# Optimization experiments

Hardware: AMD Instinct MI355X
Metric: run time of the kernel (lower is better)

The kernel has to match this reference:

```python
import jax, jax.numpy as jnp
import numpy as np

BATCH_K = 8
CUTOFF = 0.5
NONZERO_LOSS_CUTOFF = 1.4
N, D = 8192, 128


def setup_inputs() -> dict:
    key = jax.random.key(0)
    x = jax.random.normal(key, (N, D), dtype=jnp.float32)
    # the sqrt(2 - 2*sim) distance assumes unit-norm embeddings
    x = x / jnp.linalg.norm(x, axis=1, keepdims=True)
    return {"x": x}


def _forward(x, key):
    n, d = x.shape
    k = BATCH_K
    # pairwise distances on the unit sphere
    sim = x @ x.T                                   # [n, n]
    dist = jnp.sqrt(jnp.maximum(2.0 - 2.0 * sim, 0.0))
    # clamp distance from below at cutoff (canonical distance-weighted sampling;
    # repo's clamp(max=) + torch.maxx are typos that make the original code NaN/crash)
    dist = jnp.maximum(dist, CUTOFF)
    one_minus = jnp.maximum(1.0 - 0.25 * dist * dist, 1e-8)  # tiny clip for log safety
    log_w = (2.0 - float(d)) * jnp.log(dist) - (float(d - 3) / 2.0) * jnp.log(one_minus)
    w = jnp.exp(log_w - jnp.max(log_w))
    # zero out the same-class (block-diagonal) entries and far pairs
    blk = jnp.arange(n) // k
    neq_block = (blk[:, None] != blk[None, :]).astype(x.dtype)
    w = w * neq_block * (dist < NONZERO_LOSS_CUTOFF).astype(x.dtype)
    row_sum = jnp.sum(w, axis=1, keepdims=True)
    # uniform fallback for degenerate rows (mirrors the try/except in the original)
    probs = jnp.where(row_sum > 0, w / row_sum, 1.0 / n)   # [n, n]
    # per-row categorical sampling of k-1 negatives WITH replacement
    logits = jnp.log(probs)                                # -inf where prob==0 (ok)
    n_idx = jax.random.categorical(key, logits, shape=(k - 1, n)).T.reshape(-1)  # [n*(k-1)]
    # anchor/positive pairs: all same-block pairs (i, j), j != i
    a_idx = jnp.repeat(jnp.arange(n), k - 1)               # [n*(k-1)]
    p_mat = blk[:, None] * k + jnp.arange(k)[None, :]      # [n, k]
    keep = p_mat != jnp.arange(n)[:, None]
    order = jnp.argsort(jnp.logical_not(keep), axis=1, stable=True)
    p_idx = jnp.take_along_axis(p_mat, order, axis=1)[:, : k - 1].reshape(-1)
    return a_idx, x[a_idx], x[p_idx], x[n_idx], x


def reference(x):
    return _forward(x, jax.random.key(1))
```

## Files before the change

### kernel.cpp

```cpp
#include <hip/hip_runtime.h>

#define NN   8192
#define DD   128
#define KM1  7
#define TPB  256
#define NBLK 512

#define O0_END   57344
#define O1_END   7397376
#define O2_END   14737408
#define O3_END   22077440
#define TOTAL    23126016
#define NKEY     57344

typedef __attribute__((ext_vector_type(8))) short bf16x8;
typedef __attribute__((ext_vector_type(4))) float f32x4;

__device__ __forceinline__ unsigned mix32(unsigned h) {
  h ^= h >> 16; h *= 0x85ebca6bu; h ^= h >> 13; h *= 0xc2b2ae35u; h ^= h >> 16;
  return h;
}

__device__ __forceinline__ float wfun(float dot, int col, int rowblk) {
  float d2m = fmaxf(fmaf(-2.f, dot, 2.f), 0.25f);
  bool vb = ((col >> 3) != rowblk) && (d2m < 1.96f);
  float lgd = __log2f(d2m);
  float om  = fmaf(-0.25f, d2m, 1.f);
  float lgo = __log2f(om);
  float lgw = fmaf(-62.5f, lgo, fmaf(-63.f, lgd, -63.f));
  float w   = __builtin_amdgcn_exp2f(lgw);
  return vb ? w : 0.f;
}

__device__ __forceinline__ float wave_incl_scan(float v, int lane) {
#pragma unroll
  for (int off = 1; off < 64; off <<= 1) {
    float t = __shfl_up(v, off);
    if (lane >= off) v += t;
  }
  return v;
}

__global__ __launch_bounds__(256) void to_bf16(const float* __restrict__ x,
                                               unsigned short* __restrict__ xb,
                                               unsigned short* __restrict__ xbf) {
  const int c = blockIdx.x * 256 + threadIdx.x;
  const int l15 = c & 15, g = (c >> 4) & 3, kk = (c >> 6) & 3, R = c >> 8;
  const int row = R * 16 + l15;
  const int j0  = kk * 32 + g * 8;
  const float* src = x + (size_t)row * DD + j0;
  float4 a = *reinterpret_cast<const float4*>(src);
  float4 b = *reinterpret_cast<const float4*>(src + 4);
  unsigned short o[8];
  unsigned u;
  u = __float_as_uint(a.x); o[0] = (unsigned short)((u + 0x7FFFu + ((u >> 16) & 1u)) >> 16);
  u = __float_as_uint(a.y); o[1] = (unsigned short)((u + 0x7FFFu + ((u >> 16) & 1u)) >> 16);
  u = __float_as_uint(a.z); o[2] = (unsigned short)((u + 0x7FFFu + ((u >> 16) & 1u)) >> 16);
  u = __float_as_uint(a.w); o[3] = (unsigned short)((u + 0x7FFFu + ((u >> 16) & 1u)) >> 16);
  u = __float_as_uint(b.x); o[4] = (unsigned short)((u + 0x7FFFu + ((u >> 16) & 1u)) >> 16);
  u = __float_as_uint(b.y); o[5] = (unsigned short)((u + 0x7FFFu + ((u >> 16) & 1u)) >> 16);
  u = __float_as_uint(b.z); o[6] = (unsigned short)((u + 0x7FFFu + ((u >> 16) & 1u)) >> 16);
  u = __float_as_uint(b.w); o[7] = (unsigned short)((u + 0x7FFFu + ((u >> 16) & 1u)) >> 16);
  bf16x8 pk;
#pragma unroll
  for (int j = 0; j < 8; ++j) pk[j] = (short)o[j];
  *reinterpret_cast<bf16x8*>(xbf + (size_t)c * 8) = pk;
  *reinterpret_cast<bf16x8*>(xb + (size_t)row * DD + j0) = pk;
}

__global__ __launch_bounds__(TPB, 2) void pass_a(const unsigned short* __restrict__ xbf,
                                                 float* __restrict__ bs) {
  const int tid  = threadIdx.x;
  const int lane = tid & 63;
  const int wid  = tid >> 6;
  const int l15  = lane & 15;
  const int g    = lane >> 4;
  const int i0   = ((int)(blockIdx.x >> 5)) * 256 + wid * 64;
  const int oc   = (int)(blockIdx.x & 31);
  const int c0   = oc * 256;

  bf16x8 rw[4][4];
#pragma unroll
  for (int rg = 0; rg < 4; ++rg) {
    const unsigned short* rp = xbf + ((size_t)(i0 >> 4) + rg) * 2048 + lane * 8;
#pragma unroll
    for (int kk = 0; kk < 4; ++kk)
      rw[rg][kk] = *reinterpret_cast<const bf16x8*>(rp + kk * 512);
  }

  float bsl[16];
#pragma unroll
  for (int j = 0; j < 16; ++j) bsl[j] = 0.f;

#pragma unroll 1
  for (int t = 0; t < 8; ++t) {
    const int ct = c0 + t * 32;
    bf16x8 cf[2][4];
#pragma unroll
    for (int mf = 0; mf < 2; ++mf) {
      const unsigned short* cp = xbf + ((size_t)(ct >> 4) + mf) * 2048 + lane * 8;
#pragma unroll
      for (int kk = 0; kk < 4; ++kk)
        cf[mf][kk] = *reinterpret_cast<const bf16x8*>(cp + kk * 512);
    }

    f32x4 acc[2][4];
#pragma unroll
    for (int mf = 0; mf < 2; ++mf)
#pragma unroll
      for (int rg = 0; rg < 4; ++rg) acc[mf][rg] = (f32x4){0.f, 0.f, 0.f, 0.f};

#pragma unroll
    for (int mf = 0; mf < 2; ++mf)
#pragma unroll
      for (int rg = 0; rg < 4; ++rg)
#pragma unroll
        for (int kk = 0; kk < 4; ++kk)
          acc[mf][rg] = __builtin_amdgcn_mfma_f32_16x16x32_bf16(cf[mf][kk], rw[rg][kk],
                                                                acc[mf][rg], 0, 0, 0);

#pragma unroll
    for (int mf = 0; mf < 2; ++mf) {
      float s[4];
#pragma unroll
      for (int rg = 0; rg < 4; ++rg) {
        const int rowblk = (i0 + rg * 16 + l15) >> 3;
        float sv = 0.f;
#pragma unroll
        for (int r = 0; r < 4; ++r) {
          const int col = ct + mf * 16 + g * 4 + r;
          sv += wfun(acc[mf][rg][r], col, rowblk);
        }
        sv += __shfl_xor(sv, 16);
        sv += __shfl_xor(sv, 32);
        s[rg] = sv;
      }
      float v = (g == 0) ? s[0] : (g == 1) ? s[1] : (g == 2) ? s[2] : s[3];
      bsl[2 * t + mf] = v;
    }
  }

  float* dst = bs + (size_t)(i0 + lane) * NBLK + oc * 16;
#pragma unroll
  for (int k4 = 0; k4 < 4; ++k4) {
    f32x4 o = {bsl[4 * k4], bsl[4 * k4 + 1], bsl[4 * k4 + 2], bsl[4 * k4 + 3]};
    *reinterpret_cast<f32x4*>(dst + 4 * k4) = o;
  }
}

__global__ __launch_bounds__(TPB) void pass_b(const unsigned short* __restrict__ xb,
                                              const float* __restrict__ bs,
                                              unsigned* __restrict__ nidx) {
  const int lane = threadIdx.x & 63;
  const int wid  = threadIdx.x >> 6;
  const int draw = (int)blockIdx.x * 4 + wid;
  const int row  = draw / KM1;

  const float* bsr = bs + (size_t)row * NBLK;
  float4 v0 = *reinterpret_cast<const float4*>(bsr + lane * 8);
  float4 v1 = *reinterpret_cast<const float4*>(bsr + lane * 8 + 4);
  float s8 = ((v0.x + v0.y) + (v0.z + v0.w)) + ((v1.x + v1.y) + (v1.z + v1.w));
  float pre = wave_incl_scan(s8, lane);
  float W = __shfl(pre, 63);

  unsigned h = mix32((unsigned)draw * 2654435761u + 0x12345u);
  float u = ((float)(h >> 9) + 0.5f) * (1.0f / 8388608.0f);

  if (!(W > 0.f)) {
    if (lane == 0) nidx[draw] = mix32((unsigned)draw * 0x68bc21ebu + 77u) & (NN - 1);
    return;
  }
  float target = u * W;

  unsigned long long ball = __ballot(pre >= target);
  int Lc = ball ? ((int)__ffsll(ball) - 1) : 63;
  float exL = __shfl(pre - s8, Lc);
  float a0 = __shfl(v0.x, Lc), a1 = __shfl(v0.y, Lc), a2 = __shfl(v0.z, Lc),
        a3 = __shfl(v0.w, Lc), a4 = __shfl(v1.x, Lc), a5 = __shfl(v1.y, Lc),
        a6 = __shfl(v1.z, Lc), a7 = __shfl(v1.w, Lc);
  int k = -1; float res = 0.f, bsb = 0.f, c = exL;
#define PICK(j, aj) { float cn = c + (aj); if (k < 0 && cn >= target) { k = j; res = target - c; bsb = (aj); } c = cn; }
  PICK(0, a0) PICK(1, a1) PICK(2, a2) PICK(3, a3)
  PICK(4, a4) PICK(5, a5) PICK(6, a6) PICK(7, a7)
#undef PICK
#define LASTP(j, aj) { if (k < 0 && (aj) > 0.f) { k = j; res = (aj); bsb = (aj); } }
  LASTP(7, a7) LASTP(6, a6) LASTP(5, a5) LASTP(4, a4)
  LASTP(3, a3) LASTP(2, a2) LASTP(1, a1) LASTP(0, a0)
#undef LASTP
  if (k < 0) {
    if (lane == 0) nidx[draw] = mix32((unsigned)draw * 0x68bc21ebu + 77u) & (NN - 1);
    return;
  }
  const int blk = Lc * 8 + k;
  const int cb  = blk * 16;

  const int c_local = lane >> 2;
  const int part    = lane & 3;
  const int col     = cb + c_local;
  const unsigned short* cp = xb + (size_t)col * DD + part * 32;
  const unsigned short* ap = xb + (size_t)row * DD + part * 32;
  float dot = 0.f;
#pragma unroll
  for (int vv = 0; vv < 4; ++vv) {
    bf16x8 cv = *reinterpret_cast<const bf16x8*>(cp + vv * 8);
    bf16x8 av = *reinterpret_cast<const bf16x8*>(ap + vv * 8);
#pragma unroll
    for (int j = 0; j < 8; ++j) {
      float cf = __uint_as_float(((unsigned)(unsigned short)cv[j]) << 16);
      float af = __uint_as_float(((unsigned)(unsigned short)av[j]) << 16);
      dot = fmaf(cf, af, dot);
    }
  }
  dot += __shfl_xor(dot, 1);
  dot += __shfl_xor(dot, 2);
  float w = wfun(dot, col, row >> 3);
  float v = (part == 0) ? w : 0.f;
  float pre2 = wave_incl_scan(v, lane);
  float SW = __shfl(pre2, 63);
  unsigned result;
  if (SW > 0.f) {
    float t2 = (res / bsb) * SW;
    unsigned long long m = __ballot((v > 0.f) && (pre2 >= t2));
    if (m) result = (unsigned)(cb + (((int)__ffsll(m) - 1) >> 2));
    else {
      unsigned long long m2 = __ballot(v > 0.f);
      result = (unsigned)(cb + ((63 - (int)__clzll(m2)) >> 2));
    }
  } else {
    result = mix32((unsigned)draw * 0x68bc21ebu + 77u) & (NN - 1);
  }
  if (lane == 0) nidx[draw] = result;
}

__global__ __launch_bounds__(256) void write_outputs(const float* __restrict__ x,
                                                     const unsigned* __restrict__ nidx,
                                                     float* __restrict__ out) {
  const int qq = blockIdx.x * 256 + threadIdx.x;
  if (qq >= TOTAL / 4) return;
  const int e = qq * 4;
  float4 v;
  if (e < O0_END) {
    v.x = (float)((e    ) / KM1);
    v.y = (float)((e + 1) / KM1);
    v.z = (float)((e + 2) / KM1);
    v.w = (float)((e + 3) / KM1);
  } else if (e < O1_END) {
    int t = e - O0_END; int sidx = t >> 7; int d = t & 127;
    v = *reinterpret_cast<const float4*>(x + (size_t)(sidx / KM1) * DD + d);
  } else if (e < O2_END) {
    int t = e - O1_END; int sidx = t >> 7; int d = t & 127;
    int i = sidx / KM1; int j = sidx - i * KM1; int m = i & 7;
    int p = (i >> 3) * 8 + j + (j >= m ? 1 : 0);
    v = *reinterpret_cast<const float4*>(x + (size_t)p * DD + d);
  } else if (e < O3_END) {
    int t = e - O2_END; int sidx = t >> 7; int d = t & 127;
    int nix = (int)nidx[sidx];
    v = *reinterpret_cast<const float4*>(x + (size_t)nix * DD + d);
  } else {
    v = *reinterpret_cast<const float4*>(x + (e - O3_END));
  }
  f32x4 nv = {v.x, v.y, v.z, v.w};
  __builtin_nontemporal_store(nv, reinterpret_cast<f32x4*>(out + e));
}

extern "C" void kernel_launch(void* const* d_in, const int* in_sizes, int n_in,
                              void* d_out, int out_size, void* d_ws, size_t ws_size,
                              hipStream_t stream) {
  const float* x = (const float*)d_in[0];
  float* out = (float*)d_out;

  float* bs = (float*)d_ws;
  unsigned* nidx = (unsigned*)((char*)d_ws + (size_t)NN * NBLK * 4);
  unsigned short* xb  = (unsigned short*)((char*)nidx + NKEY * 4);
  unsigned short* xbf = (unsigned short*)((char*)xb + (size_t)NN * DD * 2);

  hipLaunchKernelGGL(to_bf16, dim3(NN * DD / 8 / 256), dim3(256), 0, stream, x, xb, xbf);
  hipLaunchKernelGGL(pass_a, dim3(1024), dim3(TPB), 0, stream, xbf, bs);
  hipLaunchKernelGGL(pass_b, dim3(NKEY / 4), dim3(TPB), 0, stream, xb, bs, nidx);
  hipLaunchKernelGGL(write_outputs, dim3(TOTAL / 4 / 256), dim3(256), 0, stream,
                     x, nidx, out);
}
```

Measured before the change: 105.6 us.

## Process all draws of a row in one wave in negative sampling pass

The sampling kernel now assigns one wave per row and loops over that row's seven draws. The block-sum prefix scan and the anchor row's bf16 vector are loaded and computed once per row instead of once per draw. This removes redundant global reads of the block-sum table and repeated scans. In exchange, the grid shrinks sevenfold and each wave runs a serial loop, which reduces available parallelism for hiding latency.

```diff
diff --git a/kernel.cpp b/kernel.cpp
--- a/kernel.cpp
+++ b/kernel.cpp
@@ -153,8 +153,7 @@
                                               unsigned* __restrict__ nidx) {
   const int lane = threadIdx.x & 63;
   const int wid  = threadIdx.x >> 6;
-  const int draw = (int)blockIdx.x * 4 + wid;
-  const int row  = draw / KM1;
+  const int row  = (int)blockIdx.x * 4 + wid;
 
   const float* bsr = bs + (size_t)row * NBLK;
   float4 v0 = *reinterpret_cast<const float4*>(bsr + lane * 8);
@@ -162,74 +161,98 @@
   float s8 = ((v0.x + v0.y) + (v0.z + v0.w)) + ((v1.x + v1.y) + (v1.z + v1.w));
   float pre = wave_incl_scan(s8, lane);
   float W = __shfl(pre, 63);
-
-  unsigned h = mix32((unsigned)draw * 2654435761u + 0x12345u);
-  float u = ((float)(h >> 9) + 0.5f) * (1.0f / 8388608.0f);
-
-  if (!(W > 0.f)) {
-    if (lane == 0) nidx[draw] = mix32((unsigned)draw * 0x68bc21ebu + 77u) & (NN - 1);
-    return;
-  }
-  float target = u * W;
-
-  unsigned long long ball = __ballot(pre >= target);
-  int Lc = ball ? ((int)__ffsll(ball) - 1) : 63;
-  float exL = __shfl(pre - s8, Lc);
-  float a0 = __shfl(v0.x, Lc), a1 = __shfl(v0.y, Lc), a2 = __shfl(v0.z, Lc),
-        a3 = __shfl(v0.w, Lc), a4 = __shfl(v1.x, Lc), a5 = __shfl(v1.y, Lc),
-        a6 = __shfl(v1.z, Lc), a7 = __shfl(v1.w, Lc);
-  int k = -1; float res = 0.f, bsb = 0.f, c = exL;
+  float ex = pre - s8;
+
+  const int c_local = lane >> 2;
+  const int part    = lane & 3;
+  const unsigned short* ap = xb + (size_t)row * DD + part * 32;
+  bf16x8 av0 = *reinterpret_cast<const bf16x8*>(ap);
+  bf16x8 av1 = *reinterpret_cast<const bf16x8*>(ap + 8);
+  bf16x8 av2 = *reinterpret_cast<const bf16x8*>(ap + 16);
+  bf16x8 av3 = *reinterpret_cast<const bf16x8*>(ap + 24);
+  const int rowblk = row >> 3;
+
+#pragma unroll 1
+  for (int s = 0; s < KM1; ++s) {
+    const int draw = row * KM1 + s;
+    unsigned result;
+    unsigned h = mix32((unsigned)draw * 2654435761u + 0x12345u);
+    float u = ((float)(h >> 9) + 0.5f) * (1.0f / 8388608.0f);
+
+    if (!(W > 0.f)) {
+      result = mix32((unsigned)draw * 0x68bc21ebu + 77u) & (NN - 1);
+      if (lane == 0) nidx[draw] = result;
+      continue;
+    }
+    float target = u * W;
+
+    unsigned long long ball = __ballot(pre >= target);
+    int Lc = ball ? ((int)__ffsll(ball) - 1) : 63;
+    float exL = __shfl(ex, Lc);
+    float a0 = __shfl(v0.x, Lc), a1 = __shfl(v0.y, Lc), a2 = __shfl(v0.z, Lc),
+          a3 = __shfl(v0.w, Lc), a4 = __shfl(v1.x, Lc), a5 = __shfl(v1.y, Lc),
+          a6 = __shfl(v1.z, Lc), a7 = __shfl(v1.w, Lc);
+    int k = -1; float res = 0.f, bsb = 0.f, c = exL;
 #define PICK(j, aj) { float cn = c + (aj); if (k < 0 && cn >= target) { k = j; res = target - c; bsb = (aj); } c = cn; }
-  PICK(0, a0) PICK(1, a1) PICK(2, a2) PICK(3, a3)
-  PICK(4, a4) PICK(5, a5) PICK(6, a6) PICK(7, a7)
+    PICK(0, a0) PICK(1, a1) PICK(2, a2) PICK(3, a3)
+    PICK(4, a4) PICK(5, a5) PICK(6, a6) PICK(7, a7)
 #undef PICK
 #define LASTP(j, aj) { if (k < 0 && (aj) > 0.f) { k = j; res = (aj); bsb = (aj); } }
-  LASTP(7, a7) LASTP(6, a6) LASTP(5, a5) LASTP(4, a4)
-  LASTP(3, a3) LASTP(2, a2) LASTP(1, a1) LASTP(0, a0)
+    LASTP(7, a7) LASTP(6, a6) LASTP(5, a5) LASTP(4, a4)
+    LASTP(3, a3) LASTP(2, a2) LASTP(1, a1) LASTP(0, a0)
 #undef LASTP
-  if (k < 0) {
-    if (lane == 0) nidx[draw] = mix32((unsigned)draw * 0x68bc21ebu + 77u) & (NN - 1);
-    return;
-  }
-  const int blk = Lc * 8 + k;
-  const int cb  = blk * 16;
-
-  const int c_local = lane >> 2;
-  const int part    = lane & 3;
-  const int col     = cb + c_local;
-  const unsigned short* cp = xb + (size_t)col * DD + part * 32;
-  const unsigned short* ap = xb + (size_t)row * DD + part * 32;
-  float dot = 0.f;
-#pragma unroll
-  for (int vv = 0; vv < 4; ++vv) {
-    bf16x8 cv = *reinterpret_cast<const bf16x8*>(cp + vv * 8);
-    bf16x8 av = *reinterpret_cast<const bf16x8*>(ap + vv * 8);
-#pragma unroll
-    for (int j = 0; j < 8; ++j) {
-      float cf = __uint_as_float(((unsigned)(unsigned short)cv[j]) << 16);
-      float af = __uint_as_float(((unsigned)(unsigned short)av[j]) << 16);
-      dot = fmaf(cf, af, dot);
-    }
-  }
-  dot += __shfl_xor(dot, 1);
-  dot += __shfl_xor(dot, 2);
-  float w = wfun(dot, col, row >> 3);
-  float v = (part == 0) ? w : 0.f;
-  float pre2 = wave_incl_scan(v, lane);
-  float SW = __shfl(pre2, 63);
-  unsigned result;
-  if (SW > 0.f) {
-    float t2 = (res / bsb) * SW;
-    unsigned long long m = __ballot((v > 0.f) && (pre2 >= t2));
-    if (m) result = (unsigned)(cb + (((int)__ffsll(m) - 1) >> 2));
-    else {
-      unsigned long long m2 = __ballot(v > 0.f);
-      result = (unsigned)(cb + ((63 - (int)__clzll(m2)) >> 2));
-    }
-  } else {
-    result = mix32((unsigned)draw * 0x68bc21ebu + 77u) & (NN - 1);
-  }
-  if (lane == 0) nidx[draw] = result;
+    if (k < 0) {
+      result = mix32((unsigned)draw * 0x68bc21ebu + 77u) & (NN - 1);
+      if (lane == 0) nidx[draw] = result;
+      continue;
+    }
+    const int blk = Lc * 8 + k;
+    const int cb  = blk * 16;
+
+    const int col = cb + c_local;
+    const unsigned short* cp = xb + (size_t)col * DD + part * 32;
+    float dot = 0.f;
+    {
+      bf16x8 cv = *reinterpret_cast<const bf16x8*>(cp);
+#pragma unroll
+      for (int j = 0; j < 8; ++j)
+        dot = fmaf(__uint_as_float(((unsigned)(unsigned short)cv[j]) << 16),
+                   __uint_as_float(((unsigned)(unsigned short)av0[j]) << 16), dot);
+      cv = *reinterpret_cast<const bf16x8*>(cp + 8);
+#pragma unroll
+      for (int j = 0; j < 8; ++j)
+        dot = fmaf(__uint_as_float(((unsigned)(unsigned short)cv[j]) << 16),
+                   __uint_as_float(((unsigned)(unsigned short)av1[j]) << 16), dot);
+      cv = *reinterpret_cast<const bf16x8*>(cp + 16);
+#pragma unroll
+      for (int j = 0; j < 8; ++j)
+        dot = fmaf(__uint_as_float(((unsigned)(unsigned short)cv[j]) << 16),
+                   __uint_as_float(((unsigned)(unsigned short)av2[j]) << 16), dot);
+      cv = *reinterpret_cast<const bf16x8*>(cp + 24);
+#pragma unroll
+      for (int j = 0; j < 8; ++j)
+        dot = fmaf(__uint_as_float(((unsigned)(unsigned short)cv[j]) << 16),
+                   __uint_as_float(((unsigned)(unsigned short)av3[j]) << 16), dot);
+    }
+    dot += __shfl_xor(dot, 1);
+    dot += __shfl_xor(dot, 2);
+    float w = wfun(dot, col, rowblk);
+    float v = (part == 0) ? w : 0.f;
+    float pre2 = wave_incl_scan(v, lane);
+    float SW = __shfl(pre2, 63);
+    if (SW > 0.f) {
+      float t2 = (res / bsb) * SW;
+      unsigned long long m = __ballot((v > 0.f) && (pre2 >= t2));
+      if (m) result = (unsigned)(cb + (((int)__ffsll(m) - 1) >> 2));
+      else {
+        unsigned long long m2 = __ballot(v > 0.f);
+        result = (unsigned)(cb + ((63 - (int)__clzll(m2)) >> 2));
+      }
+    } else {
+      result = mix32((unsigned)draw * 0x68bc21ebu + 77u) & (NN - 1);
+    }
+    if (lane == 0) nidx[draw] = result;
+  }
 }
 
 __global__ __launch_bounds__(256) void write_outputs(const float* __restrict__ x,
@@ -276,7 +299,7 @@
 
   hipLaunchKernelGGL(to_bf16, dim3(NN * DD / 8 / 256), dim3(256), 0, stream, x, xb, xbf);
   hipLaunchKernelGGL(pass_a, dim3(1024), dim3(TPB), 0, stream, xbf, bs);
-  hipLaunchKernelGGL(pass_b, dim3(NKEY / 4), dim3(TPB), 0, stream, xb, bs, nidx);
+  hipLaunchKernelGGL(pass_b, dim3(NN / 4), dim3(TPB), 0, stream, xb, bs, nidx);
   hipLaunchKernelGGL(write_outputs, dim3(TOTAL / 4 / 256), dim3(256), 0, stream,
                      x, nidx, out);
 }
```

Result: faster. 103.4 us (-2.1%).
